# Performance work log

Hardware: AMD Instinct MI355X
Metric: run time of the kernel (lower is better)

## Reference

```python
import jax, jax.numpy as jnp
import numpy as np

HEAD_K_DIM = 128  # linear_key_head_dim (not derivable from weight shapes alone)
EPS_NORM = 1e-6


def _l2norm(x, eps=1e-6):
    return x * jax.lax.rsqrt(jnp.sum(x * x, axis=-1, keepdims=True) + eps)


def setup_inputs() -> dict:
    key = jax.random.key(0)
    ks = jax.random.split(key, 9)
    B, S, H = 2, 1024, 2048
    Hv, Hk, Dk, Dv, K = 32, 16, 128, 128, 4
    key_dim, value_dim = Hk * Dk, Hv * Dv
    C = 2 * key_dim + value_dim  # conv_dim = 8192
    s = 0.02
    return {
        "hidden_states": jax.random.normal(ks[0], (B, S, H), jnp.float32),
        "conv_state": jnp.zeros((B, C, K - 1), jnp.float32),
        "recurrent_state": jnp.zeros((B, Hv, Dk, Dv), jnp.float32),
        "W_qkv": (jax.random.normal(ks[1], (C, H)) * s).astype(jnp.float32),
        "W_z": (jax.random.normal(ks[2], (value_dim, H)) * s).astype(jnp.float32),
        "W_b": (jax.random.normal(ks[3], (Hv, H)) * s).astype(jnp.float32),
        "W_a": (jax.random.normal(ks[4], (Hv, H)) * s).astype(jnp.float32),
        "conv_w": (jax.random.normal(ks[5], (C, K)) * s).astype(jnp.float32),
        "dt_bias": jnp.ones((Hv,), jnp.float32),
        "A_log": jnp.log(jax.random.uniform(ks[6], (Hv,), jnp.float32, 1e-3, 16.0)),
        "norm_weight": jnp.ones((Dv,), jnp.float32),
        "W_out": (jax.random.normal(ks[7], (H, value_dim)) * s).astype(jnp.float32),
    }


def reference(hidden_states, conv_state, recurrent_state, W_qkv, W_z, W_b, W_a,
              conv_w, dt_bias, A_log, norm_weight, W_out):
    B, S, H = hidden_states.shape
    Hv = dt_bias.shape[0]
    Dv = norm_weight.shape[0]
    C, K = conv_w.shape
    value_dim = Hv * Dv
    key_dim = (C - value_dim) // 2
    Dk = HEAD_K_DIM
    Hk = key_dim // Dk

    # input projections
    mixed_qkv = jnp.einsum('bsh,ch->bcs', hidden_states, W_qkv)  # (B, C, S)
    z = hidden_states @ W_z.T                                    # (B, S, value_dim)
    b = hidden_states @ W_b.T                                    # (B, S, Hv)
    a = hidden_states @ W_a.T                                    # (B, S, Hv)

    # causal depthwise conv over time with cached prefix state
    padded = jnp.concatenate([conv_state, mixed_qkv], axis=-1)   # (B, C, K-1+S)
    conv_out = sum(padded[:, :, k:k + S] * conv_w[:, k][None, :, None]
                   for k in range(K))                            # (B, C, S)
    conv_state_new = padded[:, :, -(K - 1):]
    mixed = jnp.swapaxes(jax.nn.silu(conv_out), 1, 2)            # (B, S, C)

    q = mixed[..., :key_dim].reshape(B, S, Hk, Dk)
    k = mixed[..., key_dim:2 * key_dim].reshape(B, S, Hk, Dk)
    v = mixed[..., 2 * key_dim:].reshape(B, S, Hv, Dv)

    beta = jax.nn.sigmoid(b)                                     # (B, S, Hv)
    g = -jnp.exp(A_log) * jax.nn.softplus(a + dt_bias)           # (B, S, Hv)

    rep = Hv // Hk
    if rep > 1:
        q = jnp.repeat(q, rep, axis=2)
        k = jnp.repeat(k, rep, axis=2)

    scale = Dk ** (-0.5)
    q = _l2norm(q) * scale
    k = _l2norm(k)

    # time-leading for scan: (S, B, Hv, ...)
    qT, kT, vT = (jnp.moveaxis(x, 1, 0) for x in (q, k, v))
    gT, betaT = jnp.moveaxis(g, 1, 0), jnp.moveaxis(beta, 1, 0)

    def step(state, xs):
        q_t, k_t, v_t, g_t, beta_t = xs
        state = state * jnp.exp(g_t)[..., None, None]            # decay
        kv_mem = jnp.einsum('bhk,bhkv->bhv', k_t, state)         # read
        delta = (v_t - kv_mem) * beta_t[..., None]               # correction
        state = state + jnp.einsum('bhk,bhv->bhkv', k_t, delta)  # write
        out_t = jnp.einsum('bhk,bhkv->bhv', q_t, state)          # readout
        return state, out_t

    final_state, outs = jax.lax.scan(step, recurrent_state.astype(jnp.float32),
                                     (qT, kT, vT, gT, betaT))
    core = jnp.moveaxis(outs, 0, 1)                              # (B, S, Hv, Dv)

    # gated RMS norm per value head
    var = jnp.mean(core * core, axis=-1, keepdims=True)
    xn = core * jax.lax.rsqrt(var + EPS_NORM) * norm_weight
    gated = xn * jax.nn.silu(z.reshape(B, S, Hv, Dv))

    output = gated.reshape(B, S, value_dim) @ W_out.T            # (B, S, H)
    return output, conv_state_new, final_state
```

## Files before the change

### kernel.cpp

```cpp
#include <hip/hip_runtime.h>
#include <cstdint>
#include <cstddef>

#define B_ 2
#define S_ 1024
#define H_ 2048
#define HV_ 32
#define HK_ 16
#define DK_ 128
#define DV_ 128
#define CC_ 8192
#define KEYDIM_ 2048
#define VALDIM_ 4096
#define NC_ 16
#define CS_ 64
#define NBIG 12416

typedef __attribute__((ext_vector_type(8))) short bf16x8;
typedef __attribute__((ext_vector_type(4))) float f32x4;

__device__ __forceinline__ ushort f2bf_rne(float x) {
  union { float f; uint32_t u; } c; c.f = x;
  uint32_t u = c.u + 0x7FFFu + ((c.u >> 16) & 1u);
  return (ushort)(u >> 16);
}

__device__ __forceinline__ void gld16(const void* g, void* l) {
  __builtin_amdgcn_global_load_lds(
      (const __attribute__((address_space(1))) void*)g,
      (__attribute__((address_space(3))) void*)l, 16, 0, 0);
}

__global__ void f2bf_kernel(const float* __restrict__ in, ushort* __restrict__ out, int n) {
  int i = (blockIdx.x * 256 + threadIdx.x) * 4;
  if (i >= n) return;
  float4 v = *(const float4*)(in + i);
  ushort4 o;
  o.x = f2bf_rne(v.x); o.y = f2bf_rne(v.y);
  o.z = f2bf_rne(v.z); o.w = f2bf_rne(v.w);
  *(ushort4*)(out + i) = o;
}

__global__ void wcat_kernel(const float* __restrict__ Wqkv, const float* __restrict__ Wz,
                            const float* __restrict__ Wb, const float* __restrict__ Wa,
                            ushort* __restrict__ out) {
  int i = (blockIdx.x * 256 + threadIdx.x) * 4;
  if (i >= NBIG * H_) return;
  int n = i >> 11;
  int k = i & (H_ - 1);
  float4 v = make_float4(0.f, 0.f, 0.f, 0.f);
  if (n < 8192)       v = *(const float4*)(Wqkv + (size_t)n * H_ + k);
  else if (n < 12288) v = *(const float4*)(Wz + (size_t)(n - 8192) * H_ + k);
  else if (n < 12320) v = *(const float4*)(Wb + (size_t)(n - 12288) * H_ + k);
  else if (n < 12352) v = *(const float4*)(Wa + (size_t)(n - 12320) * H_ + k);
  ushort4 o;
  o.x = f2bf_rne(v.x); o.y = f2bf_rne(v.y);
  o.z = f2bf_rne(v.z); o.w = f2bf_rne(v.w);
  *(ushort4*)(out + i) = o;
}

__device__ __forceinline__ void stage_tile(
    const ushort* aS0, const ushort* aS1, const ushort* bS0, const ushort* bS1,
    ushort* ldsA, ushort* ldsB, int wave, int k0)
{
  #pragma unroll
  for (int h = 0; h < 2; h++) {
    gld16(aS0 + k0 + h * 32, ldsA + h * 4096 + (wave * 2 + 0) * 512);
    gld16(aS1 + k0 + h * 32, ldsA + h * 4096 + (wave * 2 + 1) * 512);
    gld16(bS0 + k0 + h * 32, ldsB + h * 4096 + (wave * 2 + 0) * 512);
    gld16(bS1 + k0 + h * 32, ldsB + h * 4096 + (wave * 2 + 1) * 512);
  }
}

__global__ __launch_bounds__(256) void gemm_bf16_nt(
    const ushort* __restrict__ A, const ushort* __restrict__ B,
    float* __restrict__ C, int M, int N, int K)
{
  __shared__ ushort sL[2][2][8192];
  int t = threadIdx.x;
  int wave = t >> 6, lane = t & 63;
  int wm = wave >> 1, wn = wave & 1;
  int lrow = lane & 15, quad = lane >> 4;
  int mt = blockIdx.x, nt = blockIdx.y;

  f32x4 acc[4][4];
  #pragma unroll
  for (int i = 0; i < 4; i++)
    #pragma unroll
    for (int j = 0; j < 4; j++)
      #pragma unroll
      for (int r = 0; r < 4; r++) acc[i][j][r] = 0.f;

  const ushort* aS0 = A + (size_t)(mt * 128 + (wave * 2 + 0) * 16 + lrow) * K + quad * 8;
  const ushort* aS1 = A + (size_t)(mt * 128 + (wave * 2 + 1) * 16 + lrow) * K + quad * 8;
  const ushort* bS0 = B + (size_t)(nt * 128 + (wave * 2 + 0) * 16 + lrow) * K + quad * 8;
  const ushort* bS1 = B + (size_t)(nt * 128 + (wave * 2 + 1) * 16 + lrow) * K + quad * 8;

  stage_tile(aS0, aS1, bS0, bS1, &sL[0][0][0], &sL[0][1][0], wave, 0);
  __syncthreads();

  const int NK = K >> 6;
  for (int it = 0; it < NK; it++) {
    if (it + 1 < NK)
      stage_tile(aS0, aS1, bS0, bS1,
                 &sL[(it + 1) & 1][0][0], &sL[(it + 1) & 1][1][0],
                 wave, (it + 1) * 64);
    const ushort* bufA = &sL[it & 1][0][0];
    const ushort* bufB = &sL[it & 1][1][0];
    #pragma unroll
    for (int h = 0; h < 2; h++) {
      bf16x8 af[4], bfr[4];
      #pragma unroll
      for (int i = 0; i < 4; i++)
        af[i] = *(const bf16x8*)(bufA + h * 4096 + (wm * 4 + i) * 512 + lane * 8);
      #pragma unroll
      for (int j = 0; j < 4; j++)
        bfr[j] = *(const bf16x8*)(bufB + h * 4096 + (wn * 4 + j) * 512 + lane * 8);
      #pragma unroll
      for (int i = 0; i < 4; i++)
        #pragma unroll
        for (int j = 0; j < 4; j++)
          acc[i][j] = __builtin_amdgcn_mfma_f32_16x16x32_bf16(af[i], bfr[j], acc[i][j], 0, 0, 0);
    }
    __syncthreads();
  }

  #pragma unroll
  for (int i = 0; i < 4; i++) {
    int m_base = mt * 128 + wm * 64 + i * 16 + quad * 4;
    #pragma unroll
    for (int j = 0; j < 4; j++) {
      int n = nt * 128 + wn * 64 + j * 16 + lrow;
      #pragma unroll
      for (int rr = 0; rr < 4; rr++)
        C[(size_t)(m_base + rr) * N + n] = acc[i][j][rr];
    }
  }
}

__global__ void convstate_kernel(const float* __restrict__ Cbig,
                                 float* __restrict__ out)
{
  int idx = blockIdx.x * blockDim.x + threadIdx.x;
  if (idx >= B_ * CC_ * 3) return;
  int j = idx % 3;
  int c = (idx / 3) % CC_;
  int b = idx / (3 * CC_);
  out[idx] = Cbig[((size_t)(b * S_ + (S_ - 3 + j))) * NBIG + c];
}

__global__ __launch_bounds__(128) void prep_qkv(
    const float* __restrict__ Cbig, const float* __restrict__ conv_state,
    const float* __restrict__ conv_w,
    float* __restrict__ Qn, float* __restrict__ Kn, float* __restrict__ Vb)
{
  int group = blockIdx.x, s = blockIdx.y, b = blockIdx.z;
  int t = threadIdx.x;
  int c = group * 128 + t;
  float acc = 0.f;
  #pragma unroll
  for (int kk = 0; kk < 4; kk++) {
    int sp = s - 3 + kk;
    float x = (sp < 0) ? conv_state[((size_t)(b * CC_ + c)) * 3 + (3 + sp)]
                       : Cbig[((size_t)(b * S_ + sp)) * NBIG + c];
    acc += conv_w[c * 4 + kk] * x;
  }
  float val = acc / (1.f + __expf(-acc));

  if (group < 32) {
    __shared__ float red2[2];
    float p = val * val;
    #pragma unroll
    for (int off = 32; off > 0; off >>= 1) p += __shfl_xor(p, off);
    if ((t & 63) == 0) red2[t >> 6] = p;
    __syncthreads();
    float r = rsqrtf(red2[0] + red2[1] + 1e-6f);
    if (group < 16) {
      r *= 0.08838834764831845f;
      Qn[(((size_t)(b * HK_ + group)) * S_ + s) * DK_ + t] = val * r;
    } else {
      Kn[(((size_t)(b * HK_ + (group - 16))) * S_ + s) * DK_ + t] = val * r;
    }
  } else {
    Vb[(((size_t)(b * HV_ + (group - 32))) * S_ + s) * DV_ + t] = val;
  }
}

__global__ void prep_gb(const float* __restrict__ Cbig,
                        const float* __restrict__ A_log, const float* __restrict__ dt_bias,
                        float* __restrict__ g_buf, float* __restrict__ beta_buf)
{
  int idx = blockIdx.x * blockDim.x + threadIdx.x;
  if (idx >= B_ * HV_ * S_) return;
  int s = idx & (S_ - 1);
  int hv = (idx >> 10) & 31;
  int b = idx >> 15;
  float bv = Cbig[((size_t)(b * S_ + s)) * NBIG + 12288 + hv];
  float av = Cbig[((size_t)(b * S_ + s)) * NBIG + 12320 + hv];
  float x = av + dt_bias[hv];
  float sp = (x > 20.f) ? x : log1pf(__expf(x));
  g_buf[idx] = -__expf(A_log[hv]) * sp;
  beta_buf[idx] = 1.f / (1.f + __expf(-bv));
}

__device__ __forceinline__ int swf4(int r, int f) { return r * 32 + (f ^ (r & 31)); }
__device__ __forceinline__ int swf1(int r, int k) {
  return r * 128 + 4 * ((k >> 2) ^ (r & 31)) + (k & 3);
}

__global__ __launch_bounds__(256) void cp_kernel(
    const float* __restrict__ Qn, const float* __restrict__ Kn,
    const float* __restrict__ Vb,
    const float* __restrict__ g_buf, const float* __restrict__ beta_buf,
    float* __restrict__ G_buf, float* __restrict__ M_buf,
    float* __restrict__ KcD, float* __restrict__ D0p)
{
  __shared__ float sK[64 * 128];
  __shared__ float sX[32 * 128];
  __shared__ float sT[64 * 64];
  float* sG  = sT;
  float* sBe = sT + 64;
  float* sA  = sX;
  float* tTw = sX;
  float* tTb = sX;
  float4* sK4 = (float4*)sK;
  float4* sX4 = (float4*)sX;

  const int ch = blockIdx.x;
  const int bh = ch / NC_, c = ch % NC_;
  const int b = bh >> 5, hv = bh & 31, hk = hv >> 1;
  const int s0 = c * CS_;
  const int t = threadIdx.x;
  const size_t gOff = (size_t)bh * S_ + s0;

  float Gw0 = 0.f, Bw0 = 0.f;
  if (t < 64) {
    float gi = g_buf[gOff + t];
    Gw0 = gi;
    #pragma unroll
    for (int off = 1; off < 64; off <<= 1) {
      float o = __shfl_up(Gw0, off);
      if (t >= off) Gw0 += o;
    }
    G_buf[gOff + t] = Gw0;
    sG[t] = Gw0;
    Bw0 = beta_buf[gOff + t];
    sBe[t] = Bw0;
  }
  {
    const float4* src = (const float4*)(Kn + ((size_t)(b * HK_ + hk) * S_ + s0) * DK_);
    #pragma unroll
    for (int u = 0; u < 8; u++) {
      int idx = u * 256 + t;
      sK4[swf4(idx >> 5, idx & 31)] = src[idx];
    }
  }
  __syncthreads();

  const float4* qsrc = (const float4*)(Qn + ((size_t)(b * HK_ + hk) * S_ + s0) * DK_);
  {
    int ti2 = t >> 4, tj = t & 15;
    for (int h = 0; h < 2; h++) {
      #pragma unroll
      for (int u = 0; u < 4; u++) {
        int idx = u * 256 + t;
        sX4[swf4(idx >> 5, idx & 31)] = qsrc[h * 1024 + idx];
      }
      __syncthreads();
      float accM[2][4];
      #pragma unroll
      for (int a = 0; a < 2; a++)
        #pragma unroll
        for (int e = 0; e < 4; e++) accM[a][e] = 0.f;
      for (int k4 = 0; k4 < 32; k4++) {
        float4 qv[2], kv[4];
        qv[0] = sX4[swf4(ti2, k4)];
        qv[1] = sX4[swf4(ti2 + 16, k4)];
        #pragma unroll
        for (int e = 0; e < 4; e++) kv[e] = sK4[swf4(tj + 16 * e, k4)];
        #pragma unroll
        for (int a = 0; a < 2; a++)
          #pragma unroll
          for (int e = 0; e < 4; e++)
            accM[a][e] += qv[a].x * kv[e].x + qv[a].y * kv[e].y +
                          qv[a].z * kv[e].z + qv[a].w * kv[e].w;
      }
      #pragma unroll
      for (int a = 0; a < 2; a++) {
        int iG = h * 32 + ti2 + 16 * a;
        float Gi = sG[iG];
        #pragma unroll
        for (int e = 0; e < 4; e++) {
          int j = tj + 16 * e;
          float m = (j <= iG) ? __expf(Gi - sG[j]) * accM[a][e] : 0.f;
          M_buf[(size_t)ch * 4096 + iG * 64 + j] = m;
        }
      }
      __syncthreads();
    }
  }

  {
    int ti = t >> 4, tj = t & 15;
    float accA[4][4];
    #pragma unroll
    for (int a = 0; a < 4; a++)
      #pragma unroll
      for (int e = 0; e < 4; e++) accA[a][e] = 0.f;
    for (int k4 = 0; k4 < 32; k4++) {
      float4 ki[4], kj[4];
      #pragma unroll
      for (int e = 0; e < 4; e++) {
        ki[e] = sK4[swf4(ti + 16 * e, k4)];
        kj[e] = sK4[swf4(tj + 16 * e, k4)];
      }
      #pragma unroll
      for (int a = 0; a < 4; a++)
        #pragma unroll
        for (int e = 0; e < 4; e++)
          accA[a][e] += ki[a].x * kj[e].x + ki[a].y * kj[e].y +
                        ki[a].z * kj[e].z + ki[a].w * kj[e].w;
    }
    float resA[4][4];
    #pragma unroll
    for (int a = 0; a < 4; a++) {
      int i = ti + 16 * a;
      float Gi = sG[i], Bi = sBe[i];
      #pragma unroll
      for (int e = 0; e < 4; e++) {
        int j = tj + 16 * e;
        resA[a][e] = (j < i) ? Bi * __expf(Gi - sG[j]) * accA[a][e] : 0.f;
      }
    }
    __syncthreads();
    #pragma unroll
    for (int a = 0; a < 4; a++)
      #pragma unroll
      for (int e = 0; e < 4; e++)
        sA[(ti + 16 * a) * 64 + (tj + 16 * e)] = resA[a][e];
  }
  __syncthreads();

  if (t < 64) {
    sT[t] = (t == 0) ? 1.f : 0.f;
    for (int i = 1; i < 64; i++) {
      float acc = 0.f;
      for (int j = 0; j < i; j++) acc += sA[i * 64 + j] * sT[j * 64 + t];
      sT[i * 64 + t] = ((t == i) ? 1.f : 0.f) - acc;
    }
    float w = Bw0 * __expf(Gw0);
    for (int j = 0; j < 64; j++) {
      float wj = __shfl(w, j);
      tTw[j * 64 + t] = sT[t * 64 + j] * wj;
    }
  }
  __syncthreads();

  {
    int i04 = t >> 4, tk = t & 15;
    float accK[4][8];
    #pragma unroll
    for (int r = 0; r < 4; r++)
      #pragma unroll
      for (int u = 0; u < 8; u++) accK[r][u] = 0.f;
    for (int j = 0; j < 64; j++) {
      float4 tw = ((float4*)tTw)[j * 16 + i04];
      #pragma unroll
      for (int u = 0; u < 8; u++) {
        float kv = sK[swf1(j, tk + 16 * u)];
        accK[0][u] += tw.x * kv; accK[1][u] += tw.y * kv;
        accK[2][u] += tw.z * kv; accK[3][u] += tw.w * kv;
      }
    }
    size_t base = (size_t)ch * NBIG;
    #pragma unroll
    for (int r = 0; r < 4; r++)
      #pragma unroll
      for (int u = 0; u < 8; u++)
        KcD[base + (i04 * 4 + r) * 128 + tk + 16 * u] = accK[r][u];
  }
  __syncthreads();

  if (t < 64) {
    for (int j = 0; j < 64; j++) {
      float bj = __shfl(Bw0, j);
      tTb[j * 64 + t] = sT[t * 64 + j] * bj;
    }
  }
  {
    const float4* src = (const float4*)(Vb + ((size_t)bh * S_ + s0) * DV_);
    #pragma unroll
    for (int u = 0; u < 8; u++) {
      int idx = u * 256 + t;
      sK4[swf4(idx >> 5, idx & 31)] = src[idx];
    }
  }
  __syncthreads();

  {
    int i04 = t >> 4, tv_ = t & 15;
    float accD[4][8];
    #pragma unroll
    for (int r = 0; r < 4; r++)
      #pragma unroll
      for (int u = 0; u < 8; u++) accD[r][u] = 0.f;
    for (int j = 0; j < 64; j++) {
      float4 tb = ((float4*)tTb)[j * 16 + i04];
      #pragma unroll
      for (int u = 0; u < 8; u++) {
        float vv = sK[swf1(j, tv_ + 16 * u)];
        accD[0][u] += tb.x * vv; accD[1][u] += tb.y * vv;
        accD[2][u] += tb.z * vv; accD[3][u] += tb.w * vv;
      }
    }
    size_t base = (size_t)ch * NBIG;
    #pragma unroll
    for (int r = 0; r < 4; r++)
      #pragma unroll
      for (int u = 0; u < 8; u++)
        D0p[base + (i04 * 4 + r) * 128 + tv_ + 16 * u] = accD[r][u];
  }
}

__global__ __launch_bounds__(256) void phaseb_kernel(
    const float* __restrict__ rec_state, const float* __restrict__ Qn,
    const float* __restrict__ Kn, const float* __restrict__ G_buf,
    float* __restrict__ KcD, const float* __restrict__ D0p,
    float* __restrict__ Oq_buf, float* __restrict__ final_state)
{
  __shared__ float sS[128 * 32];
  __shared__ float sKT[128 * 64];
  __shared__ float sQT[128 * 64];
  __shared__ float sD[64 * 32];

  const int blk = blockIdx.x;
  const int bh = (blk & 7) | ((blk >> 5) << 3);
  const int vq = (blk >> 3) & 3;
  const int b = bh >> 5, hv = bh & 31, hk = hv >> 1;
  const int t = threadIdx.x;
  const int vbase = vq * 32;
  const float* gG = G_buf + (size_t)bh * S_;

  #pragma unroll
  for (int u = 0; u < 4; u++) {
    int idx = u * 256 + t;
    int k = idx >> 3;
    int v4 = (idx & 7) * 4;
    *(float4*)(&sS[k * 32 + v4]) =
        *(const float4*)(&rec_state[((size_t)bh * 128 + k) * 128 + vbase + v4]);
  }
  __syncthreads();

  const int si = t & 63, skq = t >> 6;
  const int ti = t >> 3;
  const int tv = t & 7;
  const int tk = t >> 3;

  for (int c = 0; c < NC_; c++) {
    const size_t ch = (size_t)bh * NC_ + c;
    const int s0 = c * CS_;
    const float GC = gG[s0 + 63];
    const float eGC = __expf(GC);

    {
      float eGi = __expf(gG[s0 + si]);
      const float* kcRow = KcD + ch * NBIG + si * 128 + skq * 32;
      const float* qRow  = Qn + ((size_t)(b * HK_ + hk) * S_ + s0 + si) * DK_ + skq * 32;
      #pragma unroll
      for (int u = 0; u < 8; u++) {
        float4 kc = *(const float4*)(kcRow + u * 4);
        float4 qv = *(const float4*)(qRow + u * 4);
        int kk = skq * 32 + u * 4;
        sKT[(kk + 0) * 64 + si] = kc.x; sKT[(kk + 1) * 64 + si] = kc.y;
        sKT[(kk + 2) * 64 + si] = kc.z; sKT[(kk + 3) * 64 + si] = kc.w;
        sQT[(kk + 0) * 64 + si] = qv.x * eGi; sQT[(kk + 1) * 64 + si] = qv.y * eGi;
        sQT[(kk + 2) * 64 + si] = qv.z * eGi; sQT[(kk + 3) * 64 + si] = qv.w * eGi;
      }
    }
    __syncthreads();

    {
      float accD[2][4], accO[2][4];
      #pragma unroll
      for (int r = 0; r < 2; r++) {
        float4 d0 = *(const float4*)(&D0p[ch * NBIG + (size_t)(ti * 2 + r) * 128 + vbase + tv * 4]);
        accD[r][0] = d0.x; accD[r][1] = d0.y; accD[r][2] = d0.z; accD[r][3] = d0.w;
        accO[r][0] = accO[r][1] = accO[r][2] = accO[r][3] = 0.f;
      }
      for (int k = 0; k < 128; k++) {
        float2 kc = *(const float2*)(&sKT[k * 64 + ti * 2]);
        float2 qb = *(const float2*)(&sQT[k * 64 + ti * 2]);
        float4 sv = *(const float4*)(&sS[k * 32 + tv * 4]);
        accD[0][0] -= kc.x * sv.x; accD[0][1] -= kc.x * sv.y;
        accD[0][2] -= kc.x * sv.z; accD[0][3] -= kc.x * sv.w;
        accD[1][0] -= kc.y * sv.x; accD[1][1] -= kc.y * sv.y;
        accD[1][2] -= kc.y * sv.z; accD[1][3] -= kc.y * sv.w;
        accO[0][0] += qb.x * sv.x; accO[0][1] += qb.x * sv.y;
        accO[0][2] += qb.x * sv.z; accO[0][3] += qb.x * sv.w;
        accO[1][0] += qb.y * sv.x; accO[1][1] += qb.y * sv.y;
        accO[1][2] += qb.y * sv.z; accO[1][3] += qb.y * sv.w;
      }
      #pragma unroll
      for (int r = 0; r < 2; r++) {
        int i = ti * 2 + r;
        float4 dv = make_float4(accD[r][0], accD[r][1], accD[r][2], accD[r][3]);
        float4 ov = make_float4(accO[r][0], accO[r][1], accO[r][2], accO[r][3]);
        *(float4*)(&sD[i * 32 + tv * 4]) = dv;
        *(float4*)(&KcD[ch * NBIG + (size_t)i * 128 + vbase + tv * 4]) = dv;
        *(float4*)(&Oq_buf[ch * 8192 + (size_t)i * 128 + vbase + tv * 4]) = ov;
      }
    }
    __syncthreads();

    {
      float sc = __expf(GC - gG[s0 + si]);
      const float* kRow = Kn + ((size_t)(b * HK_ + hk) * S_ + s0 + si) * DK_ + skq * 32;
      #pragma unroll
      for (int u = 0; u < 8; u++) {
        float4 x = *(const float4*)(kRow + u * 4);
        x.x *= sc; x.y *= sc; x.z *= sc; x.w *= sc;
        int kg = skq * 8 + u;
        *(float4*)(&sKT[si * 128 + 4 * (kg ^ (si & 31))]) = x;
      }
    }
    __syncthreads();

    {
      float acc[4][4];
      #pragma unroll
      for (int r = 0; r < 4; r++)
        acc[r][0] = acc[r][1] = acc[r][2] = acc[r][3] = 0.f;
      for (int i = 0; i < 64; i++) {
        float4 d  = *(const float4*)(&sD[i * 32 + tv * 4]);
        float4 ka = *(const float4*)(&sKT[i * 128 + 4 * (tk ^ (i & 31))]);
        acc[0][0] += ka.x * d.x; acc[0][1] += ka.x * d.y;
        acc[0][2] += ka.x * d.z; acc[0][3] += ka.x * d.w;
        acc[1][0] += ka.y * d.x; acc[1][1] += ka.y * d.y;
        acc[1][2] += ka.y * d.z; acc[1][3] += ka.y * d.w;
        acc[2][0] += ka.z * d.x; acc[2][1] += ka.z * d.y;
        acc[2][2] += ka.z * d.z; acc[2][3] += ka.z * d.w;
        acc[3][0] += ka.w * d.x; acc[3][1] += ka.w * d.y;
        acc[3][2] += ka.w * d.z; acc[3][3] += ka.w * d.w;
      }
      #pragma unroll
      for (int r = 0; r < 4; r++) {
        int k = tk * 4 + r;
        float4 s = *(const float4*)(&sS[k * 32 + tv * 4]);
        s.x = s.x * eGC + acc[r][0]; s.y = s.y * eGC + acc[r][1];
        s.z = s.z * eGC + acc[r][2]; s.w = s.w * eGC + acc[r][3];
        *(float4*)(&sS[k * 32 + tv * 4]) = s;
      }
    }
    __syncthreads();
  }

  #pragma unroll
  for (int u = 0; u < 4; u++) {
    int idx = u * 256 + t;
    int k = idx >> 3;
    int v4 = (idx & 7) * 4;
    *(float4*)(&final_state[((size_t)bh * 128 + k) * 128 + vbase + v4]) =
        *(const float4*)(&sS[k * 32 + v4]);
  }
}

__global__ __launch_bounds__(128) void phasec_kernel(
    const float* __restrict__ KcD, const float* __restrict__ Oq_buf,
    const float* __restrict__ M_buf, const float* __restrict__ norm_weight,
    const float* __restrict__ Cbig, ushort* __restrict__ zg_bf)
{
  __shared__ float sM[4096];
  __shared__ float red[2][2];
  int ch = blockIdx.x;
  int bh = ch / NC_, c = ch % NC_;
  int b = bh >> 5, hv = bh & 31;
  int s0 = c * CS_;
  int v = threadIdx.x;

  float Dr[64];
  #pragma unroll
  for (int j = 0; j < 64; j++) Dr[j] = KcD[(size_t)ch * NBIG + j * 128 + v];
  {
    const float4* src = (const float4*)(M_buf + (size_t)ch * 4096);
    #pragma unroll
    for (int u = 0; u < 8; u++) ((float4*)sM)[u * 128 + v] = src[u * 128 + v];
  }
  __syncthreads();
  float nw = norm_weight[v];

  for (int i = 0; i < 64; i++) {
    float o = Oq_buf[(size_t)ch * 8192 + i * 128 + v];
    const float4* mr = (const float4*)(sM + i * 64);
    #pragma unroll
    for (int j4 = 0; j4 < 16; j4++) {
      float4 m = mr[j4];
      o += m.x * Dr[4 * j4] + m.y * Dr[4 * j4 + 1] +
           m.z * Dr[4 * j4 + 2] + m.w * Dr[4 * j4 + 3];
    }
    float p = o * o;
    #pragma unroll
    for (int off = 32; off > 0; off >>= 1) p += __shfl_xor(p, off);
    if ((v & 63) == 0) red[i & 1][v >> 6] = p;
    __syncthreads();
    float var = (red[i & 1][0] + red[i & 1][1]) * (1.f / 128.f);
    float xn = o * rsqrtf(var + 1e-6f) * nw;
    float zv = Cbig[((size_t)(b * S_ + s0 + i)) * NBIG + 8192 + hv * DV_ + v];
    zg_bf[((size_t)(b * S_ + s0 + i)) * VALDIM_ + hv * DV_ + v] =
        f2bf_rne(xn * (zv / (1.f + __expf(-zv))));
  }
}

extern "C" void kernel_launch(void* const* d_in, const int* in_sizes, int n_in,
                              void* d_out, int out_size, void* d_ws, size_t ws_size,
                              hipStream_t stream)
{
  const float* hs          = (const float*)d_in[0];
  const float* conv_state  = (const float*)d_in[1];
  const float* rec_state   = (const float*)d_in[2];
  const float* W_qkv       = (const float*)d_in[3];
  const float* W_z         = (const float*)d_in[4];
  const float* W_b         = (const float*)d_in[5];
  const float* W_a         = (const float*)d_in[6];
  const float* conv_w      = (const float*)d_in[7];
  const float* dt_bias     = (const float*)d_in[8];
  const float* A_log       = (const float*)d_in[9];
  const float* norm_weight = (const float*)d_in[10];
  const float* W_out       = (const float*)d_in[11];

  float* out       = (float*)d_out;
  float* out_conv  = out + (size_t)B_ * S_ * H_;
  float* out_state = out_conv + (size_t)B_ * CC_ * 3;

  float* ws = (float*)d_ws;
  float* Cbig = ws;
  float* KcD  = Cbig;
  float* D0p  = Cbig + (size_t)1024 * NBIG;
  float* g_buf    = ws + 25427968;
  float* beta_buf = ws + 25493504;
  float* G_buf    = ws + 25559040;
  float* Qn       = ws + 25624576;
  float* Kn       = ws + 29818880;
  float* Vb       = ws + 34013184;
  float* M_buf    = ws + 42401792;
  float* Oq_buf   = Vb;

  ushort* Wcat_bf = (ushort*)(ws + 25427968);
  ushort* hs_bf   = (ushort*)(ws + 38141952);
  ushort* zg_bf   = (ushort*)Qn;
  ushort* Wout_bf = (ushort*)Kn;

  const int M = B_ * S_;

  f2bf_kernel<<<(M * H_) / 1024, 256, 0, stream>>>(hs, hs_bf, M * H_);
  wcat_kernel<<<(NBIG * H_) / 1024, 256, 0, stream>>>(W_qkv, W_z, W_b, W_a, Wcat_bf);
  gemm_bf16_nt<<<dim3(M / 128, NBIG / 128), 256, 0, stream>>>(hs_bf, Wcat_bf, Cbig, M, NBIG, H_);
  convstate_kernel<<<(B_ * CC_ * 3 + 255) / 256, 256, 0, stream>>>(Cbig, out_conv);
  prep_qkv<<<dim3(64, S_, B_), 128, 0, stream>>>(Cbig, conv_state, conv_w, Qn, Kn, Vb);
  prep_gb<<<(B_ * HV_ * S_ + 255) / 256, 256, 0, stream>>>(Cbig, A_log, dt_bias, g_buf, beta_buf);
  cp_kernel<<<B_ * HV_ * NC_, 256, 0, stream>>>(Qn, Kn, Vb, g_buf, beta_buf,
                                                G_buf, M_buf, KcD, D0p);
  phaseb_kernel<<<B_ * HV_ * 4, 256, 0, stream>>>(rec_state, Qn, Kn, G_buf,
                                                  KcD, D0p, Oq_buf, out_state);
  f2bf_kernel<<<(H_ * VALDIM_) / 1024, 256, 0, stream>>>(W_out, Wout_bf, H_ * VALDIM_);
  phasec_kernel<<<B_ * HV_ * NC_, 128, 0, stream>>>(KcD, Oq_buf, M_buf,
                                                    norm_weight, Cbig, zg_bf);
  gemm_bf16_nt<<<dim3(M / 128, H_ / 128), 256, 0, stream>>>(zg_bf, Wout_bf, out, M, H_, VALDIM_);
}
```

Before: 988.0 us.

## Use 256x256-tile 8-wave pipelined bf16 GEMM for fused input projection

Adds a new GEMM kernel with 256x256 output tiles, 512 threads and double-buffered LDS, staged in four interleaved phases with explicit vmcnt waits, barriers and setprio around the MFMA blocks. It replaces the 128x128 GEMM for the big input projection. The concatenated weight is padded to a multiple of 256 rows and the hidden-state bf16 buffer is moved to make room. The larger tiles aim to raise data reuse per LDS load and hide global loads behind MFMA work. The cost is higher register and LDS pressure and fewer blocks in the grid.

New measurement: 952.9 us. 1.04x faster.

```diff
diff --git a/kernel.cpp b/kernel.cpp
--- a/kernel.cpp
+++ b/kernel.cpp
@@ -15,6 +15,7 @@
 #define NC_ 16
 #define CS_ 64
 #define NBIG 12416
+#define NBIGP 12544
 
 typedef __attribute__((ext_vector_type(8))) short bf16x8;
 typedef __attribute__((ext_vector_type(4))) float f32x4;
@@ -45,7 +46,7 @@
                             const float* __restrict__ Wb, const float* __restrict__ Wa,
                             ushort* __restrict__ out) {
   int i = (blockIdx.x * 256 + threadIdx.x) * 4;
-  if (i >= NBIG * H_) return;
+  if (i >= NBIGP * H_) return;
   int n = i >> 11;
   int k = i & (H_ - 1);
   float4 v = make_float4(0.f, 0.f, 0.f, 0.f);
@@ -57,6 +58,125 @@
   o.x = f2bf_rne(v.x); o.y = f2bf_rne(v.y);
   o.z = f2bf_rne(v.z); o.w = f2bf_rne(v.w);
   *(ushort4*)(out + i) = o;
+}
+
+#define MEMF() asm volatile("" ::: "memory")
+#define VMW(n) asm volatile("s_waitcnt vmcnt(" #n ")" ::: "memory")
+#define BARR() do { __builtin_amdgcn_s_barrier(); MEMF(); } while (0)
+
+#define ST(P, SHM, RG, o, kq) do {                                  \
+    gld16((P) + (kq),      &SHM[o][((RG) * 2 + 0) * 512]);          \
+    gld16((P) + (kq) + 32, &SHM[o][((RG) * 2 + 1) * 512]);          \
+  } while (0)
+
+#define LDA(ah, c) do { _Pragma("unroll")                                            \
+    for (int i_ = 0; i_ < 4; i_++) { _Pragma("unroll")                               \
+      for (int h_ = 0; h_ < 2; h_++)                                                 \
+        aF[i_ * 2 + h_] = *(const bf16x8*)(                                          \
+            &sAm[c][((wm * 8 + (ah) * 4 + i_) * 2 + h_) * 512 + lane * 8]); } } while (0)
+
+#define LDB(dst, bh, c) do { _Pragma("unroll")                                       \
+    for (int j_ = 0; j_ < 2; j_++) { _Pragma("unroll")                               \
+      for (int h_ = 0; h_ < 2; h_++)                                                 \
+        dst[j_ * 2 + h_] = *(const bf16x8*)(                                         \
+            &sBm[c][((wn * 4 + (bh) * 2 + j_) * 2 + h_) * 512 + lane * 8]); } } while (0)
+
+#define MM(ah, bh, bsrc) do {                                                        \
+    __builtin_amdgcn_s_setprio(1);                                                   \
+    _Pragma("unroll") for (int h_ = 0; h_ < 2; h_++)                                 \
+    _Pragma("unroll") for (int i_ = 0; i_ < 4; i_++)                                 \
+    _Pragma("unroll") for (int j_ = 0; j_ < 2; j_++)                                 \
+      acc[(ah) * 4 + i_][(bh) * 2 + j_] = __builtin_amdgcn_mfma_f32_16x16x32_bf16(   \
+          aF[i_ * 2 + h_], bsrc[j_ * 2 + h_], acc[(ah) * 4 + i_][(bh) * 2 + j_],     \
+          0, 0, 0);                                                                  \
+    __builtin_amdgcn_s_setprio(0);                                                   \
+  } while (0)
+
+__global__ __launch_bounds__(512, 2) void gemm256_8ph(
+    const ushort* __restrict__ A, const ushort* __restrict__ B,
+    float* __restrict__ C, int Ns, int K)
+{
+  __shared__ ushort sAm[2][16384];
+  __shared__ ushort sBm[2][16384];
+
+  const int t = threadIdx.x;
+  const int wave = t >> 6, lane = t & 63;
+  const int wm = wave >> 2, wn = wave & 3;
+  const int l15 = lane & 15, l4 = lane >> 4;
+  const int mt = blockIdx.x, nt = blockIdx.y;
+
+  const int rgS0 = (wave & 3) + (wave >> 2) * 8;
+  const int rgS3 = rgS0 + 4;
+  const int rgS1 = (wave & 1) + (wave >> 1) * 4;
+  const int rgS2 = rgS1 + 2;
+
+  const ushort* aP0 = A + (size_t)(mt * 256 + rgS0 * 16 + l15) * K + l4 * 8;
+  const ushort* aP1 = A + (size_t)(mt * 256 + rgS3 * 16 + l15) * K + l4 * 8;
+  const ushort* bP0 = B + (size_t)(nt * 256 + rgS1 * 16 + l15) * K + l4 * 8;
+  const ushort* bP1 = B + (size_t)(nt * 256 + rgS2 * 16 + l15) * K + l4 * 8;
+
+  f32x4 acc[8][4];
+  #pragma unroll
+  for (int i = 0; i < 8; i++)
+    #pragma unroll
+    for (int j = 0; j < 4; j++)
+      #pragma unroll
+      for (int r = 0; r < 4; r++) acc[i][j][r] = 0.f;
+
+  bf16x8 aF[8], bF0[4], bF1[4];
+
+  ST(aP0, sAm, rgS0, 0, 0); MEMF();
+  ST(bP0, sBm, rgS1, 0, 0); MEMF();
+  ST(bP1, sBm, rgS2, 0, 0); MEMF();
+  ST(aP1, sAm, rgS3, 0, 0); MEMF();
+
+  const int NT = K >> 6;
+  for (int tt = 0; tt < NT - 1; tt++) {
+    const int c = tt & 1, o = c ^ 1;
+    const int kq = (tt + 1) << 6;
+    VMW(4); BARR();
+    ST(aP0, sAm, rgS0, o, kq);
+    LDA(0, c); LDB(bF0, 0, c);
+    MM(0, 0, bF0);
+    VMW(4); BARR();
+    ST(bP0, sBm, rgS1, o, kq);
+    LDB(bF1, 1, c);
+    MM(0, 1, bF1);
+    VMW(4); BARR();
+    ST(bP1, sBm, rgS2, o, kq);
+    LDA(1, c);
+    MM(1, 1, bF1);
+    MEMF();
+    ST(aP1, sAm, rgS3, o, kq);
+    MM(1, 0, bF0);
+  }
+  {
+    const int c = (NT - 1) & 1;
+    VMW(4); BARR();
+    LDA(0, c); LDB(bF0, 0, c);
+    MM(0, 0, bF0);
+    VMW(2); BARR();
+    LDB(bF1, 1, c);
+    MM(0, 1, bF1);
+    VMW(0); BARR();
+    LDA(1, c);
+    MM(1, 1, bF1);
+    MM(1, 0, bF0);
+  }
+
+  #pragma unroll
+  for (int mf = 0; mf < 8; mf++) {
+    const int row0 = mt * 256 + wm * 128 + mf * 16 + l4 * 4;
+    #pragma unroll
+    for (int nf = 0; nf < 4; nf++) {
+      const int col = nt * 256 + wn * 64 + nf * 16 + l15;
+      if (col < Ns) {
+        #pragma unroll
+        for (int r = 0; r < 4; r++)
+          C[(size_t)(row0 + r) * Ns + col] = acc[mf][nf][r];
+      }
+    }
+  }
 }
 
 __device__ __forceinline__ void stage_tile(
@@ -645,15 +765,15 @@
   float* Oq_buf   = Vb;
 
   ushort* Wcat_bf = (ushort*)(ws + 25427968);
-  ushort* hs_bf   = (ushort*)(ws + 38141952);
+  ushort* hs_bf   = (ushort*)(ws + 38273024);
   ushort* zg_bf   = (ushort*)Qn;
   ushort* Wout_bf = (ushort*)Kn;
 
   const int M = B_ * S_;
 
   f2bf_kernel<<<(M * H_) / 1024, 256, 0, stream>>>(hs, hs_bf, M * H_);
-  wcat_kernel<<<(NBIG * H_) / 1024, 256, 0, stream>>>(W_qkv, W_z, W_b, W_a, Wcat_bf);
-  gemm_bf16_nt<<<dim3(M / 128, NBIG / 128), 256, 0, stream>>>(hs_bf, Wcat_bf, Cbig, M, NBIG, H_);
+  wcat_kernel<<<(NBIGP * H_) / 1024, 256, 0, stream>>>(W_qkv, W_z, W_b, W_a, Wcat_bf);
+  gemm256_8ph<<<dim3(M / 256, NBIGP / 256), 512, 0, stream>>>(hs_bf, Wcat_bf, Cbig, NBIG, H_);
   convstate_kernel<<<(B_ * CC_ * 3 + 255) / 256, 256, 0, stream>>>(Cbig, out_conv);
   prep_qkv<<<dim3(64, S_, B_), 128, 0, stream>>>(Cbig, conv_state, conv_w, Qn, Kn, Vb);
   prep_gb<<<(B_ * HV_ * S_ + 255) / 256, 256, 0, stream>>>(Cbig, A_log, dt_bias, g_buf, beta_buf);
```
